# Performance work log

Hardware: AMD Instinct MI355X
Metric: run time of the kernel (lower is better)

Reference implementation:

```python
import jax, jax.numpy as jnp
import numpy as np

HEADS = 8
DIM_HEAD = 128
H = 32
W = 32
SCALE = DIM_HEAD ** (-0.5)


def rel_to_abs(x):
    # x: (b, nh, l, 2l-1) -> (b, nh, l, l) via pad/reshape trick
    b, nh, l, _ = x.shape
    x = jnp.pad(x, ((0, 0), (0, 0), (0, 0), (0, 1)))            # (b,nh,l,2l)
    flat = x.reshape(b, nh, l * 2 * l)
    flat = jnp.pad(flat, ((0, 0), (0, 0), (0, l - 1)))
    final = flat.reshape(b, nh, l + 1, 2 * l - 1)
    return final[:, :, :l, l - 1:]


def relative_logits_1d(q, rel_k):
    # q: (b,n,h,w,d), rel_k: (2w-1,d) -> (b,n,h,h,w,w)
    b, n, h, w, d = q.shape
    logits = jnp.einsum('bnhwd,rd->bnhwr', q, rel_k)
    logits = logits.reshape(b, n * h, w, 2 * w - 1)
    logits = rel_to_abs(logits).reshape(b, n, h, w, w)
    return jnp.broadcast_to(logits[:, :, :, None], (b, n, h, h, w, w))


def rel_pos_logits(q, rel_height, rel_width):
    # q: (b,n,h*w,d) -> (b,n,h*w,h*w)
    b, n, _, d = q.shape
    qh = q.reshape(b, n, H, W, d)
    # width logits: 'b n h H w W -> b n (h w) (H W)'
    rw = relative_logits_1d(qh, rel_width)                       # (b,n,h,H,w,W)
    rw = jnp.transpose(rw, (0, 1, 2, 4, 3, 5)).reshape(b, n, H * W, H * W)
    # height logits: q transposed to (b,n,w,h,d); result 'b n w W h H'
    qt = jnp.transpose(qh, (0, 1, 3, 2, 4))
    rh = relative_logits_1d(qt, rel_height)                      # (b,n,w,W,h,H)
    rh = jnp.transpose(rh, (0, 1, 4, 2, 5, 3)).reshape(b, n, H * W, H * W)
    return rw + rh


def setup_inputs() -> dict:
    key = jax.random.key(0)
    k1, k2, k3, k4 = jax.random.split(key, 4)
    featuremap = jax.random.normal(k1, (8, 512, H, W), dtype=jnp.float32)
    w_qkv = jax.random.normal(k2, (3 * HEADS * DIM_HEAD, 512), dtype=jnp.float32) * 0.02
    rel_height = jax.random.normal(k3, (2 * H - 1, DIM_HEAD), dtype=jnp.float32) * SCALE
    rel_width = jax.random.normal(k4, (2 * W - 1, DIM_HEAD), dtype=jnp.float32) * SCALE
    return {"featuremap": featuremap, "w_qkv": w_qkv,
            "rel_height": rel_height, "rel_width": rel_width}


def reference(featuremap, w_qkv, rel_height, rel_width):
    b, c, h, w = featuremap.shape
    n, d = HEADS, DIM_HEAD
    qkv = jnp.einsum('oc,bchw->bohw', w_qkv, featuremap)         # 1x1 conv, no bias
    q, k, v = jnp.split(qkv, 3, axis=1)

    def to_heads(t):  # 'b (n d) h w -> b n (h w) d'
        return jnp.transpose(t.reshape(b, n, d, h * w), (0, 1, 3, 2))

    q, k, v = to_heads(q), to_heads(k), to_heads(v)
    q = q * SCALE
    logits = jnp.einsum('bnxd,bnyd->bnxy', q, k)
    logits = logits + rel_pos_logits(q, rel_height, rel_width)
    weights = jax.nn.softmax(logits, axis=-1)
    attn_out = jnp.einsum('bnxy,bnyd->bnxd', weights, v)         # (b,n,hw,d)
    # 'b n (h w) d -> b (n d) h w'
    return jnp.transpose(attn_out, (0, 1, 3, 2)).reshape(b, n * d, h, w)
```

## Files before the change

### kernel.cpp

```cpp
#include <hip/hip_runtime.h>

#define BATCH 8
#define CIN   512
#define NH    8
#define DH    128
#define PP    1024
#define QK_SCALE 0.08838834764831845f

typedef unsigned int  u32;
typedef unsigned short u16;
typedef __attribute__((ext_vector_type(8)))  short short8;
typedef __attribute__((ext_vector_type(16))) float f32x16;

typedef __attribute__((address_space(1))) const u32 GU32;
typedef __attribute__((address_space(3))) u32 LU32;


__device__ inline u32 f2bf(float x) {
    u32 u = __float_as_uint(x);
    return (u + 0x7fffu + ((u >> 16) & 1u)) >> 16;
}
__device__ inline float bf2f(u32 h) { return __uint_as_float(h << 16); }

__device__ inline void cvt8(const float* v, float scl, uint4& hv, uint4& lv) {
    u32 h[8], l[8];
#pragma unroll
    for (int j = 0; j < 8; ++j) {
        float x = v[j] * scl;
        u32 hb = f2bf(x);
        float hf = bf2f(hb);
        u32 lb = f2bf(x - hf);
        h[j] = hb; l[j] = lb;
    }
    hv = make_uint4(h[0] | (h[1] << 16), h[2] | (h[3] << 16),
                    h[4] | (h[5] << 16), h[6] | (h[7] << 16));
    lv = make_uint4(l[0] | (l[1] << 16), l[2] | (l[3] << 16),
                    l[4] | (l[5] << 16), l[6] | (l[7] << 16));
}

__global__ __launch_bounds__(256) void wconv(
    const float* __restrict__ w, char* __restrict__ AIMG)
{
    const int gid = blockIdx.x * 256 + threadIdx.x;
    const int o  = gid >> 6;
    const int c0 = (gid & 63) << 3;
    const float scl = (o < 1024) ? QK_SCALE : 1.0f;
    float v[8];
    float4 v0 = *(const float4*)(w + (size_t)o * CIN + c0);
    float4 v1 = *(const float4*)(w + (size_t)o * CIN + c0 + 4);
    v[0]=v0.x; v[1]=v0.y; v[2]=v0.z; v[3]=v0.w;
    v[4]=v1.x; v[5]=v1.y; v[6]=v1.z; v[7]=v1.w;
    uint4 hv, lv; cvt8(v, scl, hv, lv);
    const int otile = o >> 7, row = o & 127, chunk = c0 >> 5, g = (c0 >> 3) & 3;
    char* base = AIMG + (size_t)(otile * 16 + chunk) * 16384
               + row * 64 + ((g ^ (row & 3)) << 4);
    *(uint4*)(base)        = hv;
    *(uint4*)(base + 8192) = lv;
}

__global__ __launch_bounds__(256) void fmconv(
    const float* __restrict__ fm, char* __restrict__ FIMG)
{
    __shared__ float Fs[32][128];
    const int t = threadIdx.x;
    const int chunk = blockIdx.x, ptile = blockIdx.y, b = blockIdx.z;
    const float* src = fm + ((size_t)(b * CIN + chunk * 32)) * PP + ptile * 128;
#pragma unroll
    for (int ii = 0; ii < 4; ++ii) {
        int idx = t + 256 * ii;
        int c = idx >> 5, p4 = idx & 31;
        *(float4*)(&Fs[c][p4 * 4]) = *(const float4*)(src + (size_t)c * PP + p4 * 4);
    }
    __syncthreads();
    const int p = t & 127, gb = (t >> 7) * 2;
#pragma unroll
    for (int gi = 0; gi < 2; ++gi) {
        const int g = gb + gi;
        float v[8];
#pragma unroll
        for (int j = 0; j < 8; ++j) v[j] = Fs[g * 8 + j][p];
        uint4 hv, lv; cvt8(v, 1.0f, hv, lv);
        char* base = FIMG + (size_t)((b * 8 + ptile) * 16 + chunk) * 16384
                   + p * 64 + ((g ^ (p & 3)) << 4);
        *(uint4*)(base)        = hv;
        *(uint4*)(base + 8192) = lv;
    }
}

__global__ __launch_bounds__(256) void relprep(
    const float* __restrict__ relH, const float* __restrict__ relW,
    char* __restrict__ RELIMG)
{
    const int idx = blockIdx.x * 256 + threadIdx.x;
    const int r = idx >> 4, g = idx & 15;
    float v[8];
    if (r < 63) {
        float4 v0 = *(const float4*)(relH + (size_t)r * DH + g * 8);
        float4 v1 = *(const float4*)(relH + (size_t)r * DH + g * 8 + 4);
        v[0]=v0.x; v[1]=v0.y; v[2]=v0.z; v[3]=v0.w;
        v[4]=v1.x; v[5]=v1.y; v[6]=v1.z; v[7]=v1.w;
    } else if (r < 126) {
        float4 v0 = *(const float4*)(relW + (size_t)(r - 63) * DH + g * 8);
        float4 v1 = *(const float4*)(relW + (size_t)(r - 63) * DH + g * 8 + 4);
        v[0]=v0.x; v[1]=v0.y; v[2]=v0.z; v[3]=v0.w;
        v[4]=v1.x; v[5]=v1.y; v[6]=v1.z; v[7]=v1.w;
    } else {
#pragma unroll
        for (int j = 0; j < 8; ++j) v[j] = 0.f;
    }
    uint4 hv, lv; cvt8(v, 1.0f, hv, lv);
    char* base = RELIMG + r * 256 + ((g ^ (r & 15)) << 4);
    *(uint4*)(base)         = hv;
    *(uint4*)(base + 32768) = lv;
}

__global__ __launch_bounds__(256, 2) void qkv_gemm(
    const char* __restrict__ AIMG, const char* __restrict__ FIMG,
    u16* __restrict__ Qhi, u16* __restrict__ Qlo,
    char* __restrict__ KIMG, char* __restrict__ VIMG)
{
    __shared__ char lds[65536];

    const int t = threadIdx.x, lane = t & 63, wid = t >> 6;
    const int l31 = lane & 31, h5 = lane >> 5;
    const int ptile = blockIdx.x, otile = blockIdx.y, b = blockIdx.z;
    const int wr = wid >> 1, wc = wid & 1;

    const char* Achunks = AIMG + (size_t)(otile * 16) * 16384;
    const char* Bchunks = FIMG + (size_t)((b * 8 + ptile) * 16) * 16384;

    const int half = wid & 1;
    const char* srcTile = (wid < 2) ? Achunks : Bchunks;
    char* dstBase0 = lds + ((wid < 2) ? 0 : 16384) + half * 8192;

    auto stageChunk = [&](int chunk, int par) {
        const char* src = srcTile + (size_t)chunk * 16384 + half * 8192 + lane * 16;
        char* dst = dstBase0 + par * 32768;
#pragma unroll
        for (int c = 0; c < 8; ++c)
            __builtin_amdgcn_global_load_lds((GU32*)(src + c * 1024),
                                             (LU32*)(dst + c * 1024), 16, 0, 0);
    };

    f32x16 acc[2][2];
#pragma unroll
    for (int i = 0; i < 2; ++i)
#pragma unroll
        for (int j = 0; j < 2; ++j)
#pragma unroll
            for (int r = 0; r < 16; ++r) acc[i][j][r] = 0.f;

    auto computeChunk = [&](int par) {
        const char* Abuf = lds + par * 32768;
        const char* Bbuf = Abuf + 16384;
#pragma unroll
        for (int ks = 0; ks < 2; ++ks) {
            short8 a_h[2], a_l[2], b_h[2], b_l[2];
#pragma unroll
            for (int ot = 0; ot < 2; ++ot) {
                const int row = wr * 64 + ot * 32 + l31;
                const int off = row * 64 + (((ks * 2 + h5) ^ (row & 3)) << 4);
                a_h[ot] = *(const short8*)(Abuf + off);
                a_l[ot] = *(const short8*)(Abuf + 8192 + off);
            }
#pragma unroll
            for (int pt = 0; pt < 2; ++pt) {
                const int col = wc * 64 + pt * 32 + l31;
                const int off = col * 64 + (((ks * 2 + h5) ^ (col & 3)) << 4);
                b_h[pt] = *(const short8*)(Bbuf + off);
                b_l[pt] = *(const short8*)(Bbuf + 8192 + off);
            }
#pragma unroll
            for (int ot = 0; ot < 2; ++ot)
#pragma unroll
                for (int pt = 0; pt < 2; ++pt) {
                    acc[ot][pt] = __builtin_amdgcn_mfma_f32_32x32x16_bf16(a_h[ot], b_h[pt], acc[ot][pt], 0, 0, 0);
                    acc[ot][pt] = __builtin_amdgcn_mfma_f32_32x32x16_bf16(a_h[ot], b_l[pt], acc[ot][pt], 0, 0, 0);
                    acc[ot][pt] = __builtin_amdgcn_mfma_f32_32x32x16_bf16(a_l[ot], b_h[pt], acc[ot][pt], 0, 0, 0);
                }
        }
    };

    stageChunk(0, 0);
    for (int ch = 0; ch < 15; ++ch) {
        stageChunk(ch + 1, (ch + 1) & 1);
        asm volatile("s_waitcnt vmcnt(8)" ::: "memory");
        __builtin_amdgcn_sched_barrier(0);
        __builtin_amdgcn_s_barrier();
        __builtin_amdgcn_sched_barrier(0);
        computeChunk(ch & 1);
        __builtin_amdgcn_s_barrier();
        __builtin_amdgcn_sched_barrier(0);
    }
    asm volatile("s_waitcnt vmcnt(0)" ::: "memory");
    __builtin_amdgcn_sched_barrier(0);
    __builtin_amdgcn_s_barrier();
    __builtin_amdgcn_sched_barrier(0);
    computeChunk(1);
    __syncthreads();

    float* Cs = (float*)lds;
#pragma unroll
    for (int ot = 0; ot < 2; ++ot)
#pragma unroll
        for (int pt = 0; pt < 2; ++pt)
#pragma unroll
            for (int r = 0; r < 16; ++r) {
                const int o = wr * 64 + ot * 32 + (r & 3) + 8 * (r >> 2) + 4 * h5;
                const int p = wc * 64 + pt * 32 + l31;
                Cs[o * 128 + (p ^ (o & 31))] = acc[ot][pt][r];
            }
    __syncthreads();

    const int tsel = otile >> 3;
    const int n    = otile & 7;
    const int bn   = b * NH + n;

    if (tsel == 0) {
        const int d0 = (t & 15) * 8, prow = t >> 4;
#pragma unroll
        for (int i = 0; i < 8; ++i) {
            const int p = prow + 16 * i;
            float v[8];
#pragma unroll
            for (int j = 0; j < 8; ++j)
                v[j] = Cs[(d0 + j) * 128 + (p ^ ((d0 + j) & 31))];
            uint4 hv, lv; cvt8(v, 1.0f, hv, lv);
            const size_t off = ((size_t)bn * PP + ptile * 128 + p) * DH + d0;
            *(uint4*)(Qhi + off) = hv;
            *(uint4*)(Qlo + off) = lv;
        }
    } else if (tsel == 1) {
        const int d0 = (t & 15) * 8, prow = t >> 4;
#pragma unroll
        for (int i = 0; i < 8; ++i) {
            const int p = prow + 16 * i;
            float v[8];
#pragma unroll
            for (int j = 0; j < 8; ++j)
                v[j] = Cs[(d0 + j) * 128 + (p ^ ((d0 + j) & 31))];
            uint4 hv, lv; cvt8(v, 1.0f, hv, lv);
            const int kt = ptile * 4 + (p >> 5), r32 = p & 31;
            char* base = KIMG + ((size_t)(bn * 32 + kt) << 14)
                       + r32 * 256 + (((d0 >> 3) ^ (r32 & 15)) << 4);
            *(uint4*)(base)        = hv;
            *(uint4*)(base + 8192) = lv;
        }
    } else {
        const int g = t & 3, dbase = t >> 2;
#pragma unroll
        for (int i = 0; i < 2; ++i) {
            const int d = dbase + 64 * i;
#pragma unroll
            for (int ks = 0; ks < 4; ++ks) {
                const int p0 = ks * 32 + g * 8;
                float v[8];
#pragma unroll
                for (int j = 0; j < 8; ++j)
                    v[j] = Cs[d * 128 + ((p0 + j) ^ (d & 31))];
                uint4 hv, lv; cvt8(v, 1.0f, hv, lv);
                char* base = VIMG + ((size_t)(bn * 32 + ptile * 4 + ks) << 14)
                           + d * 64 + ((g ^ (d & 3)) << 4);
                *(uint4*)(base)        = hv;
                *(uint4*)(base + 8192) = lv;
            }
        }
    }
}

__global__ __launch_bounds__(256, 1) void rel_gemm(
    const u16* __restrict__ Qhi, const u16* __restrict__ Qlo,
    const char* __restrict__ RELIMG, float* __restrict__ R)
{
    __shared__ char lds[131072];
    const int t = threadIdx.x, lane = t & 63, wid = t >> 6;
    const int l31 = lane & 31, h5 = lane >> 5;
    const int bn = blockIdx.y, p0 = blockIdx.x * 128;

    {
        const char* src = RELIMG + wid * 16384 + lane * 16;
        char* dst = lds + wid * 16384;
#pragma unroll
        for (int c = 0; c < 16; ++c)
            __builtin_amdgcn_global_load_lds((GU32*)(src + c * 1024),
                                             (LU32*)(dst + c * 1024), 16, 0, 0);
    }
#pragma unroll
    for (int pt = 0; pt < 4; ++pt) {
#pragma unroll
        for (int half = 0; half < 2; ++half) {
            const u16* srcp = (half ? Qlo : Qhi) + ((size_t)bn * PP + p0 + pt * 32) * DH;
            char* dstb = lds + 65536 + pt * 16384 + half * 8192;
#pragma unroll
            for (int ii = 0; ii < 2; ++ii) {
                const int f = t + 256 * ii;
                const int p = f >> 4, g = f & 15;
                uint4 v = *(const uint4*)((const char*)srcp + f * 16);
                *(uint4*)(dstb + p * 256 + ((g ^ (p & 15)) << 4)) = v;
            }
        }
    }
    asm volatile("s_waitcnt vmcnt(0) lgkmcnt(0)" ::: "memory");
    __builtin_amdgcn_s_barrier();
    __builtin_amdgcn_sched_barrier(0);

    f32x16 acc[4];
#pragma unroll
    for (int i = 0; i < 4; ++i)
#pragma unroll
        for (int r = 0; r < 16; ++r) acc[i][r] = 0.f;

    const int rrow = wid * 32 + l31;
#pragma unroll
    for (int kk = 0; kk < 8; ++kk) {
        const int g = kk * 2 + h5;
        const int aoff = rrow * 256 + ((g ^ (rrow & 15)) << 4);
        short8 ah = *(const short8*)(lds + aoff);
        short8 al = *(const short8*)(lds + 32768 + aoff);
        const int boff = l31 * 256 + ((g ^ (l31 & 15)) << 4);
#pragma unroll
        for (int pt = 0; pt < 4; ++pt) {
            const char* bb = lds + 65536 + pt * 16384;
            short8 bh = *(const short8*)(bb + boff);
            short8 bl = *(const short8*)(bb + 8192 + boff);
            acc[pt] = __builtin_amdgcn_mfma_f32_32x32x16_bf16(ah, bh, acc[pt], 0, 0, 0);
            acc[pt] = __builtin_amdgcn_mfma_f32_32x32x16_bf16(ah, bl, acc[pt], 0, 0, 0);
            acc[pt] = __builtin_amdgcn_mfma_f32_32x32x16_bf16(al, bh, acc[pt], 0, 0, 0);
        }
    }
    __syncthreads();

    float* Cs = (float*)lds;
#pragma unroll
    for (int pt = 0; pt < 4; ++pt)
#pragma unroll
        for (int r = 0; r < 16; ++r) {
            const int jr = wid * 32 + (r & 3) + 8 * (r >> 2) + 4 * h5;
            Cs[jr * 132 + pt * 32 + l31] = acc[pt][r];
        }
    __syncthreads();

    const int pl = t >> 1, jh = t & 1;
    const int pg = p0 + pl, hq = pg >> 5, wq = pg & 31;
    const int base = jh ? (94 - wq) : (31 - hq);
    float* dst = R + ((size_t)bn * PP + pg) * 64 + jh * 32;
#pragma unroll
    for (int j4 = 0; j4 < 8; ++j4) {
        float4 v;
        v.x = Cs[(base + j4 * 4 + 0) * 132 + pl];
        v.y = Cs[(base + j4 * 4 + 1) * 132 + pl];
        v.z = Cs[(base + j4 * 4 + 2) * 132 + pl];
        v.w = Cs[(base + j4 * 4 + 3) * 132 + pl];
        *(float4*)(dst + j4 * 4) = v;
    }
}

__global__ __launch_bounds__(256, 2) void attn_kernel(
    const u16* __restrict__ Qhi, const u16* __restrict__ Qlo,
    const char* __restrict__ KIMG, const char* __restrict__ VIMG,
    const float* __restrict__ R, float* __restrict__ out)
{
    __shared__ char lds[81920];

    const int t    = threadIdx.x;
    const int lane = t & 63, wid = t >> 6;
    const int bn = blockIdx.y, q0 = blockIdx.x * 128;
    const int b  = bn >> 3,  n = bn & 7;
    const int l31 = lane & 31, h5 = lane >> 5;
    const int q_local = wid * 32 + l31;
    const int q = q0 + q_local;

    short8 qh[8], ql[8];
    {
        const u16* qrh = Qhi + ((size_t)bn * PP + q) * DH + h5 * 8;
        const u16* qrl = Qlo + ((size_t)bn * PP + q) * DH + h5 * 8;
#pragma unroll
        for (int kk = 0; kk < 8; ++kk) {
            qh[kk] = *(const short8*)(qrh + kk * 16);
            ql[kk] = *(const short8*)(qrl + kk * 16);
        }
    }
    float R2a[16];
    {
        const float* r2p = R + ((size_t)bn * PP + q) * 64 + 32 + h5 * 4;
#pragma unroll
        for (int m_ = 0; m_ < 4; ++m_) {
            float4 v = *(const float4*)(r2p + m_ * 8);
            R2a[m_*4+0] = v.x; R2a[m_*4+1] = v.y; R2a[m_*4+2] = v.z; R2a[m_*4+3] = v.w;
        }
    }
    float* R1p = (float*)(lds + 65536);
    {
#pragma unroll
        for (int r = 0; r < 4; ++r) {
            int idx = t + 256 * r;
            int row = idx >> 3, c4 = (idx & 7) * 4;
            float4 v = *(const float4*)(R + ((size_t)bn * PP + q0 + row) * 64 + c4);
            R1p[row * 32 + ((c4 + 0) ^ (row & 31))] = v.x;
            R1p[row * 32 + ((c4 + 1) ^ (row & 31))] = v.y;
            R1p[row * 32 + ((c4 + 2) ^ (row & 31))] = v.z;
            R1p[row * 32 + ((c4 + 3) ^ (row & 31))] = v.w;
        }
    }

    auto issueK = [&](int kt, int par) {
        const char* src = KIMG + (((size_t)bn * 32 + kt) << 14) + wid * 4096 + lane * 16;
        const char* dst = lds + par * 16384 + wid * 4096;
#pragma unroll
        for (int c = 0; c < 4; ++c)
            __builtin_amdgcn_global_load_lds((GU32*)(src + c * 1024),
                                             (LU32*)(dst + c * 1024), 16, 0, 0);
    };
    auto issueV = [&](int kt) {
        const char* src = VIMG + (((size_t)bn * 32 + kt) << 14) + wid * 4096 + lane * 16;
        const char* dst = lds + 32768 + wid * 4096;
#pragma unroll
        for (int c = 0; c < 4; ++c)
            __builtin_amdgcn_global_load_lds((GU32*)(src + c * 1024),
                                             (LU32*)(dst + c * 1024), 16, 0, 0);
    };

    issueK(0, 0);
    asm volatile("s_waitcnt lgkmcnt(0)" ::: "memory");
    __builtin_amdgcn_s_barrier();
    __builtin_amdgcn_sched_barrier(0);

    f32x16 o_[4];
#pragma unroll
    for (int i = 0; i < 4; ++i)
#pragma unroll
        for (int r = 0; r < 16; ++r) o_[i][r] = 0.f;

    float m_run = -1e30f, l_run = 0.f;
    u32* Pp = (u32*)(lds + 49152 + wid * 4096);

    for (int kt = 0; kt < 32; ++kt) {
        const int par = kt & 1;
        issueV(kt);
        issueK((kt + 1) & 31, par ^ 1);
        asm volatile("s_waitcnt vmcnt(8)" ::: "memory");
        __builtin_amdgcn_sched_barrier(0);
        __builtin_amdgcn_s_barrier();
        __builtin_amdgcn_sched_barrier(0);

        f32x16 s;
#pragma unroll
        for (int r = 0; r < 16; ++r) s[r] = 0.f;
        const char* kb = lds + par * 16384;
#pragma unroll
        for (int kk = 0; kk < 8; ++kk) {
            const int g = kk * 2 + h5;
            const int off = l31 * 256 + ((g ^ (l31 & 15)) << 4);
            short8 kh = *(const short8*)(kb + off);
            short8 kl = *(const short8*)(kb + 8192 + off);
            s = __builtin_amdgcn_mfma_f32_32x32x16_bf16(kh, qh[kk], s, 0, 0, 0);
            s = __builtin_amdgcn_mfma_f32_32x32x16_bf16(kh, ql[kk], s, 0, 0, 0);
            s = __builtin_amdgcn_mfma_f32_32x32x16_bf16(kl, qh[kk], s, 0, 0, 0);
        }
        const float r1 = R1p[q_local * 32 + (kt ^ l31)];

        float mx = -1e30f;
#pragma unroll
        for (int r = 0; r < 16; ++r) {
            s[r] += R2a[r];
            mx = fmaxf(mx, s[r]);
        }
        mx = fmaxf(mx, __shfl_xor(mx, 32));
        const float pmax  = mx + r1;
        const float m_new = fmaxf(m_run, pmax);
        const float alpha = __expf(m_run - m_new);
        const float tsh   = r1 - m_new;
        float rsum = 0.f;
        u32 pw[16];
#pragma unroll
        for (int r = 0; r < 16; ++r) {
            float p = __expf(s[r] + tsh);
            rsum += p;
            u32 ph = f2bf(p);
            u32 pl = f2bf(p - bf2f(ph));
            pw[r] = (ph << 16) | pl;
        }
        rsum += __shfl_xor(rsum, 32);
        l_run = l_run * alpha + rsum;
        m_run = m_new;
#pragma unroll
        for (int r = 0; r < 16; ++r) {
            const int kr = (r & 3) + ((r >> 2) << 3) + h5 * 4;
            Pp[kr * 32 + l31] = pw[r];
        }
#pragma unroll
        for (int i = 0; i < 4; ++i)
#pragma unroll
            for (int r = 0; r < 16; ++r) o_[i][r] *= alpha;

        asm volatile("s_waitcnt vmcnt(4)" ::: "memory");
        __builtin_amdgcn_sched_barrier(0);
        __builtin_amdgcn_s_barrier();
        __builtin_amdgcn_sched_barrier(0);

        const char* vb = lds + 32768;
#pragma unroll
        for (int kk2 = 0; kk2 < 2; ++kk2) {
            u32 pu[8];
            const int kbase = kk2 * 16 + h5 * 8;
#pragma unroll
            for (int j = 0; j < 8; ++j) pu[j] = Pp[(kbase + j) * 32 + l31];
            short8 pH, pL;
#pragma unroll
            for (int j = 0; j < 8; ++j) {
                pH[j] = (short)(pu[j] >> 16);
                pL[j] = (short)(pu[j] & 0xffffu);
            }
#pragma unroll
            for (int nt = 0; nt < 4; ++nt) {
                const int d = nt * 32 + l31;
                const int g = kk2 * 2 + h5;
                const int off = d * 64 + ((g ^ (d & 3)) << 4);
                short8 vh = *(const short8*)(vb + off);
                short8 vl = *(const short8*)(vb + 8192 + off);
                o_[nt] = __builtin_amdgcn_mfma_f32_32x32x16_bf16(vh, pH, o_[nt], 0, 0, 0);
                o_[nt] = __builtin_amdgcn_mfma_f32_32x32x16_bf16(vl, pH, o_[nt], 0, 0, 0);
                o_[nt] = __builtin_amdgcn_mfma_f32_32x32x16_bf16(vh, pL, o_[nt], 0, 0, 0);
            }
        }
        __builtin_amdgcn_s_barrier();
        __builtin_amdgcn_sched_barrier(0);
    }
    asm volatile("s_waitcnt vmcnt(0)" ::: "memory");

    const float inv = 1.f / l_run;
#pragma unroll
    for (int nt = 0; nt < 4; ++nt)
#pragma unroll
        for (int r = 0; r < 16; ++r) {
            const int d = nt * 32 + (r & 3) + ((r >> 2) << 3) + h5 * 4;
            out[((size_t)b * 1024 + n * 128 + d) * PP + q] = o_[nt][r] * inv;
        }
}

extern "C" void kernel_launch(void* const* d_in, const int* in_sizes, int n_in,
                              void* d_out, int out_size, void* d_ws, size_t ws_size,
                              hipStream_t stream)
{
    const float* fm   = (const float*)d_in[0];
    const float* wqkv = (const float*)d_in[1];
    const float* relH = (const float*)d_in[2];
    const float* relW = (const float*)d_in[3];
    float* out = (float*)d_out;

    char* ws = (char*)d_ws;
    u16*  Qhi   = (u16*)(ws);
    u16*  Qlo   = (u16*)(ws + (16ull << 20));
    char* KIMG  = ws + (32ull << 20);
    char* VIMG  = ws + (64ull << 20);
    float* R    = (float*)(ws + (96ull << 20));
    char* FIMG  = ws + (96ull << 20);
    char* AIMG  = ws + (112ull << 20);
    char* RELIMG= ws + (119ull << 20);

    wconv  <<<768, 256, 0, stream>>>(wqkv, AIMG);
    fmconv <<<dim3(16, 8, 8), 256, 0, stream>>>(fm, FIMG);
    relprep<<<8, 256, 0, stream>>>(relH, relW, RELIMG);
    qkv_gemm<<<dim3(8, 24, 8), 256, 0, stream>>>(AIMG, FIMG, Qhi, Qlo, KIMG, VIMG);
    rel_gemm<<<dim3(8, 64), 256, 0, stream>>>(Qhi, Qlo, RELIMG, R);
    attn_kernel<<<dim3(8, 64), 256, 0, stream>>>(Qhi, Qlo, KIMG, VIMG, R, out);
}
```

Measured before the change: 304.9 us.

## Keep softmax probabilities in registers via permlane swap, lazy rescale, setprio, block remap

```diff
diff --git a/kernel.cpp b/kernel.cpp
--- a/kernel.cpp
+++ b/kernel.cpp
@@ -11,6 +11,7 @@
 typedef unsigned short u16;
 typedef __attribute__((ext_vector_type(8)))  short short8;
 typedef __attribute__((ext_vector_type(16))) float f32x16;
+typedef __attribute__((ext_vector_type(4)))  u32 u32x4;
 
 typedef __attribute__((address_space(1))) const u32 GU32;
 typedef __attribute__((address_space(3))) u32 LU32;
@@ -21,6 +22,17 @@
     return (u + 0x7fffu + ((u >> 16) & 1u)) >> 16;
 }
 __device__ inline float bf2f(u32 h) { return __uint_as_float(h << 16); }
+
+__device__ inline u32 cvtpk(float a, float b) {
+    u32 r; asm("v_cvt_pk_bf16_f32 %0, %1, %2" : "=v"(r) : "v"(a), "v"(b)); return r;
+}
+__device__ inline void split2(float a, float b, u32& wh, u32& wl) {
+    u32 h = cvtpk(a, b);
+    float ha = __uint_as_float(h << 16);
+    float hb = __uint_as_float(h & 0xffff0000u);
+    wl = cvtpk(a - ha, b - hb);
+    wh = h;
+}
 
 __device__ inline void cvt8(const float* v, float scl, uint4& hv, uint4& lv) {
     u32 h[8], l[8];
@@ -360,11 +372,13 @@
     const char* __restrict__ KIMG, const char* __restrict__ VIMG,
     const float* __restrict__ R, float* __restrict__ out)
 {
-    __shared__ char lds[81920];
+    __shared__ char lds[65536];
 
     const int t    = threadIdx.x;
     const int lane = t & 63, wid = t >> 6;
-    const int bn = blockIdx.y, q0 = blockIdx.x * 128;
+    const int lin = blockIdx.x;
+    const int bn  = (lin & 7) * 8 + (lin >> 6);
+    const int q0  = ((lin >> 3) & 7) * 128;
     const int b  = bn >> 3,  n = bn & 7;
     const int l31 = lane & 31, h5 = lane >> 5;
     const int q_local = wid * 32 + l31;
@@ -389,7 +403,7 @@
             R2a[m_*4+0] = v.x; R2a[m_*4+1] = v.y; R2a[m_*4+2] = v.z; R2a[m_*4+3] = v.w;
         }
     }
-    float* R1p = (float*)(lds + 65536);
+    float* R1p = (float*)(lds + 49152);
     {
 #pragma unroll
         for (int r = 0; r < 4; ++r) {
@@ -432,7 +446,6 @@
         for (int r = 0; r < 16; ++r) o_[i][r] = 0.f;
 
     float m_run = -1e30f, l_run = 0.f;
-    u32* Pp = (u32*)(lds + 49152 + wid * 4096);
 
     for (int kt = 0; kt < 32; ++kt) {
         const int par = kt & 1;
@@ -447,6 +460,7 @@
 #pragma unroll
         for (int r = 0; r < 16; ++r) s[r] = 0.f;
         const char* kb = lds + par * 16384;
+        __builtin_amdgcn_s_setprio(1);
 #pragma unroll
         for (int kk = 0; kk < 8; ++kk) {
             const int g = kk * 2 + h5;
@@ -457,6 +471,7 @@
             s = __builtin_amdgcn_mfma_f32_32x32x16_bf16(kh, ql[kk], s, 0, 0, 0);
             s = __builtin_amdgcn_mfma_f32_32x32x16_bf16(kl, qh[kk], s, 0, 0, 0);
         }
+        __builtin_amdgcn_s_setprio(0);
         const float r1 = R1p[q_local * 32 + (kt ^ l31)];
 
         float mx = -1e30f;
@@ -466,32 +481,47 @@
             mx = fmaxf(mx, s[r]);
         }
         mx = fmaxf(mx, __shfl_xor(mx, 32));
-        const float pmax  = mx + r1;
-        const float m_new = fmaxf(m_run, pmax);
-        const float alpha = __expf(m_run - m_new);
-        const float tsh   = r1 - m_new;
+        const float pmax = mx + r1;
+        if (__any(pmax > m_run + 8.0f)) {
+            const float m_new = fmaxf(m_run, pmax);
+            const float alpha = __expf(m_run - m_new);
+            l_run *= alpha;
+#pragma unroll
+            for (int i = 0; i < 4; ++i)
+#pragma unroll
+                for (int r = 0; r < 16; ++r) o_[i][r] *= alpha;
+            m_run = m_new;
+        }
+        const float tsh = r1 - m_run;
+        float pf[16];
         float rsum = 0.f;
-        u32 pw[16];
 #pragma unroll
         for (int r = 0; r < 16; ++r) {
             float p = __expf(s[r] + tsh);
             rsum += p;
-            u32 ph = f2bf(p);
-            u32 pl = f2bf(p - bf2f(ph));
-            pw[r] = (ph << 16) | pl;
+            pf[r] = p;
         }
         rsum += __shfl_xor(rsum, 32);
-        l_run = l_run * alpha + rsum;
-        m_run = m_new;
-#pragma unroll
-        for (int r = 0; r < 16; ++r) {
-            const int kr = (r & 3) + ((r >> 2) << 3) + h5 * 4;
-            Pp[kr * 32 + l31] = pw[r];
-        }
-#pragma unroll
-        for (int i = 0; i < 4; ++i)
-#pragma unroll
-            for (int r = 0; r < 16; ++r) o_[i][r] *= alpha;
+        l_run += rsum;
+
+        short8 pH[2], pL[2];
+#pragma unroll
+        for (int kk2 = 0; kk2 < 2; ++kk2) {
+            const int b8 = kk2 * 8;
+            u32 h0, l0, h1, l1, h2, l2, h3, l3;
+            split2(pf[b8 + 0], pf[b8 + 1], h0, l0);
+            split2(pf[b8 + 2], pf[b8 + 3], h1, l1);
+            split2(pf[b8 + 4], pf[b8 + 5], h2, l2);
+            split2(pf[b8 + 6], pf[b8 + 7], h3, l3);
+            asm("v_permlane32_swap_b32 %0, %1" : "+v"(h0), "+v"(h2));
+            asm("v_permlane32_swap_b32 %0, %1" : "+v"(h1), "+v"(h3));
+            asm("v_permlane32_swap_b32 %0, %1" : "+v"(l0), "+v"(l2));
+            asm("v_permlane32_swap_b32 %0, %1" : "+v"(l1), "+v"(l3));
+            u32x4 vh = {h0, h1, h2, h3};
+            u32x4 vl = {l0, l1, l2, l3};
+            pH[kk2] = __builtin_bit_cast(short8, vh);
+            pL[kk2] = __builtin_bit_cast(short8, vl);
+        }
 
         asm volatile("s_waitcnt vmcnt(4)" ::: "memory");
         __builtin_amdgcn_sched_barrier(0);
@@ -499,18 +529,9 @@
         __builtin_amdgcn_sched_barrier(0);
 
         const char* vb = lds + 32768;
+        __builtin_amdgcn_s_setprio(1);
 #pragma unroll
         for (int kk2 = 0; kk2 < 2; ++kk2) {
-            u32 pu[8];
-            const int kbase = kk2 * 16 + h5 * 8;
-#pragma unroll
-            for (int j = 0; j < 8; ++j) pu[j] = Pp[(kbase + j) * 32 + l31];
-            short8 pH, pL;
-#pragma unroll
-            for (int j = 0; j < 8; ++j) {
-                pH[j] = (short)(pu[j] >> 16);
-                pL[j] = (short)(pu[j] & 0xffffu);
-            }
 #pragma unroll
             for (int nt = 0; nt < 4; ++nt) {
                 const int d = nt * 32 + l31;
@@ -518,11 +539,12 @@
                 const int off = d * 64 + ((g ^ (d & 3)) << 4);
                 short8 vh = *(const short8*)(vb + off);
                 short8 vl = *(const short8*)(vb + 8192 + off);
-                o_[nt] = __builtin_amdgcn_mfma_f32_32x32x16_bf16(vh, pH, o_[nt], 0, 0, 0);
-                o_[nt] = __builtin_amdgcn_mfma_f32_32x32x16_bf16(vl, pH, o_[nt], 0, 0, 0);
-                o_[nt] = __builtin_amdgcn_mfma_f32_32x32x16_bf16(vh, pL, o_[nt], 0, 0, 0);
+                o_[nt] = __builtin_amdgcn_mfma_f32_32x32x16_bf16(vh, pH[kk2], o_[nt], 0, 0, 0);
+                o_[nt] = __builtin_amdgcn_mfma_f32_32x32x16_bf16(vl, pH[kk2], o_[nt], 0, 0, 0);
+                o_[nt] = __builtin_amdgcn_mfma_f32_32x32x16_bf16(vh, pL[kk2], o_[nt], 0, 0, 0);
             }
         }
+        __builtin_amdgcn_s_setprio(0);
         __builtin_amdgcn_s_barrier();
         __builtin_amdgcn_sched_barrier(0);
     }
@@ -563,5 +585,5 @@
     relprep<<<8, 256, 0, stream>>>(relH, relW, RELIMG);
     qkv_gemm<<<dim3(8, 24, 8), 256, 0, stream>>>(AIMG, FIMG, Qhi, Qlo, KIMG, VIMG);
     rel_gemm<<<dim3(8, 64), 256, 0, stream>>>(Qhi, Qlo, RELIMG, R);
-    attn_kernel<<<dim3(8, 64), 256, 0, stream>>>(Qhi, Qlo, KIMG, VIMG, R, out);
-}
+    attn_kernel<<<512, 256, 0, stream>>>(Qhi, Qlo, KIMG, VIMG, R, out);
+}
```

Result: faster. 283.8 us (-6.9%).
